# Performance work log

Hardware: AMD Instinct MI355X
Metric: run time of the kernel (lower is better)

Reference implementation:

```python
import jax, jax.numpy as jnp
import numpy as np

EPS = 1e-07

def setup_inputs() -> dict:
    key = jax.random.key(0)
    k1, k2, k3 = jax.random.split(key, 3)
    B, H, W = 32, 1024, 1024
    predictions = jax.random.uniform(k1, (B, 1, H, W), dtype=jnp.float32)
    # bboxes (x1,y1,x2,y2) normalized, with x1<x2 and y1<y2
    lo = jax.random.uniform(k2, (B, 2), dtype=jnp.float32) * 0.3        # x1,y1 in [0,0.3)
    hi = 0.6 + jax.random.uniform(k3, (B, 2), dtype=jnp.float32) * 0.4  # x2,y2 in [0.6,1.0)
    bboxes = jnp.concatenate([lo, hi], axis=1)  # [B,4]
    return {"predictions": predictions, "bboxes": bboxes}

def reference(predictions, bboxes):
    B, _, H, W = predictions.shape
    p = predictions[:, 0]  # [B,H,W]
    # int(bbox * dim) truncates; bbox >= 0 so floor matches torch's int()
    x1 = jnp.maximum(jnp.floor(bboxes[:, 0] * W).astype(jnp.int32), 0)
    y1 = jnp.maximum(jnp.floor(bboxes[:, 1] * H).astype(jnp.int32), 0)
    x2 = jnp.minimum(jnp.floor(bboxes[:, 2] * W).astype(jnp.int32), W)
    y2 = jnp.minimum(jnp.floor(bboxes[:, 3] * H).astype(jnp.int32), H)
    ys = jnp.arange(H, dtype=jnp.int32)[None, :, None]  # [1,H,1]
    xs = jnp.arange(W, dtype=jnp.int32)[None, None, :]  # [1,1,W]
    inside = ((ys >= y1[:, None, None]) & (ys < y2[:, None, None]) &
              (xs >= x1[:, None, None]) & (xs < x2[:, None, None]))  # [B,H,W]
    outside = ~inside
    per_pix = -jnp.log(1.0 - p + EPS)  # [B,H,W]
    cnt = jnp.sum(outside, axis=(1, 2)).astype(p.dtype)          # [B]
    s = jnp.sum(jnp.where(outside, per_pix, 0.0), axis=(1, 2))   # [B]
    per_sample = jnp.where(cnt > 0, s / jnp.maximum(cnt, 1.0), 0.0)
    return jnp.sum(per_sample) / B
```

## Files before the change

kernel.cpp:

```cpp
#include <hip/hip_runtime.h>
#include <math.h>

constexpr int B = 32;
constexpr int H = 1024;
constexpr int W = 1024;
constexpr int BPB  = 128;
constexpr int NBLK = B * BPB;
constexpr int RPB  = H / BPB;
constexpr int NTHREADS = 256;

__global__ __launch_bounds__(NTHREADS)
void partial_kernel(const float* __restrict__ pred,
                    const float* __restrict__ bboxes,
                    float* __restrict__ ws) {
    const int g   = blockIdx.x;
    const int b   = g & (B - 1);
    const int y0  = (g >> 5) * RPB;
    const int tid = threadIdx.x;

    const int x1 = max((int)floorf(bboxes[b * 4 + 0] * (float)W), 0);
    const int y1 = max((int)floorf(bboxes[b * 4 + 1] * (float)H), 0);
    const int x2 = min((int)floorf(bboxes[b * 4 + 2] * (float)W), W);
    const int y2 = min((int)floorf(bboxes[b * 4 + 3] * (float)H), H);

    const float area = (float)max(0, y2 - y1) * (float)max(0, x2 - x1);
    const float cnt  = (float)(H * W) - area;
    const float inv  = (cnt > 0.0f) ? (1.0f / fmaxf(cnt, 1.0f)) : 0.0f;

    const int nL   = (x1 + 3) >> 2;
    const int rS   = x2 >> 2;
    const int nAct = nL + (256 - rS);

    const float* base = pred + ((size_t)b << 20);

    float acc = 0.0f;
#pragma unroll
    for (int j = 0; j < RPB; ++j) {
        const int y = y0 + j;
        const bool yin = (y >= y1) && (y < y2);
        int c4;
        if (yin) {
            if (tid < nL)        c4 = tid;
            else if (tid < nAct) c4 = rS + (tid - nL);
            else continue;
        } else {
            c4 = tid;
        }

        const float4 v = *reinterpret_cast<const float4*>(
            base + ((size_t)y << 10) + (c4 << 2));
        const float pv[4] = {v.x, v.y, v.z, v.w};
#pragma unroll
        for (int k = 0; k < 4; ++k) {
            const int x = (c4 << 2) + k;
            const bool inside = yin && (x >= x1) && (x < x2);
            if (!inside) acc -= __logf(1.0f - pv[k] + 1e-7f);
        }
    }
    acc *= inv;

    for (int off = 32; off > 0; off >>= 1)
        acc += __shfl_down(acc, off, 64);
    __shared__ float s[NTHREADS / 64];
    const int wave = tid >> 6;
    if ((tid & 63) == 0) s[wave] = acc;
    __syncthreads();
    if (tid == 0)
        ws[g] = s[0] + s[1] + s[2] + s[3];
}

__global__ __launch_bounds__(NTHREADS)
void finalize_kernel(const float* __restrict__ ws, float* __restrict__ out) {
    const int tid = threadIdx.x;
    float t = 0.0f;
    const float* p = ws + (size_t)tid * (NBLK / NTHREADS);
#pragma unroll
    for (int i = 0; i < NBLK / NTHREADS; ++i) t += p[i];
    for (int off = 32; off > 0; off >>= 1)
        t += __shfl_down(t, off, 64);
    __shared__ float s[NTHREADS / 64];
    const int wave = tid >> 6;
    if ((tid & 63) == 0) s[wave] = t;
    __syncthreads();
    if (tid == 0)
        out[0] = (s[0] + s[1] + s[2] + s[3]) * (1.0f / (float)B);
}

extern "C" void kernel_launch(void* const* d_in, const int* in_sizes, int n_in,
                              void* d_out, int out_size, void* d_ws, size_t ws_size,
                              hipStream_t stream) {
    const float* pred   = (const float*)d_in[0];
    const float* bboxes = (const float*)d_in[1];
    float* out = (float*)d_out;
    float* ws  = (float*)d_ws;

    partial_kernel<<<NBLK, NTHREADS, 0, stream>>>(pred, bboxes, ws);
    finalize_kernel<<<1, NTHREADS, 0, stream>>>(ws, out);
}
```

Measured before the change: 24.84 us.

## Interleave rows per block and split loops into outside/inside bbox regions

```diff
diff --git a/kernel.cpp b/kernel.cpp
--- a/kernel.cpp
+++ b/kernel.cpp
@@ -4,18 +4,36 @@
 constexpr int B = 32;
 constexpr int H = 1024;
 constexpr int W = 1024;
-constexpr int BPB  = 128;
+constexpr int BPB  = 64;
+constexpr int ROWS = H / BPB;
 constexpr int NBLK = B * BPB;
-constexpr int RPB  = H / BPB;
 constexpr int NTHREADS = 256;
+constexpr int STR = BPB * W;
+
+__device__ __forceinline__ float row4(const float4 v) {
+    float s = 0.0f;
+    s -= __logf(1.0f - v.x + 1e-7f);
+    s -= __logf(1.0f - v.y + 1e-7f);
+    s -= __logf(1.0f - v.z + 1e-7f);
+    s -= __logf(1.0f - v.w + 1e-7f);
+    return s;
+}
+__device__ __forceinline__ float row4w(const float4 v, const float4 w) {
+    float s = 0.0f;
+    s -= w.x * __logf(1.0f - v.x + 1e-7f);
+    s -= w.y * __logf(1.0f - v.y + 1e-7f);
+    s -= w.z * __logf(1.0f - v.z + 1e-7f);
+    s -= w.w * __logf(1.0f - v.w + 1e-7f);
+    return s;
+}
 
 __global__ __launch_bounds__(NTHREADS)
 void partial_kernel(const float* __restrict__ pred,
                     const float* __restrict__ bboxes,
                     float* __restrict__ ws) {
     const int g   = blockIdx.x;
-    const int b   = g & (B - 1);
-    const int y0  = (g >> 5) * RPB;
+    const int b   = g >> 6;
+    const int blk = g & (BPB - 1);
     const int tid = threadIdx.x;
 
     const int x1 = max((int)floorf(bboxes[b * 4 + 0] * (float)W), 0);
@@ -27,43 +45,68 @@
     const float cnt  = (float)(H * W) - area;
     const float inv  = (cnt > 0.0f) ? (1.0f / fmaxf(cnt, 1.0f)) : 0.0f;
 
-    const int nL   = (x1 + 3) >> 2;
-    const int rS   = x2 >> 2;
-    const int nAct = nL + (256 - rS);
+    const int iLo = min(ROWS, max(0, (y1 - blk + 63) >> 6));
+    const int iHi = min(ROWS, max(iLo, (y2 - blk + 63) >> 6));
 
-    const float* base = pred + ((size_t)b << 20);
+    const float* base = pred + ((size_t)b << 20) + ((size_t)blk << 10);
+    const float* pO   = base + (tid << 2);
 
-    float acc = 0.0f;
-#pragma unroll
-    for (int j = 0; j < RPB; ++j) {
-        const int y = y0 + j;
-        const bool yin = (y >= y1) && (y < y2);
-        int c4;
-        if (yin) {
-            if (tid < nL)        c4 = tid;
-            else if (tid < nAct) c4 = rS + (tid - nL);
-            else continue;
-        } else {
-            c4 = tid;
+    float acc = 0.0f, acc2 = 0.0f;
+
+    {
+        int i = 0;
+        for (; i + 2 <= iLo; i += 2) {
+            const float4 va = *reinterpret_cast<const float4*>(pO + (size_t)i * STR);
+            const float4 vb = *reinterpret_cast<const float4*>(pO + (size_t)(i + 1) * STR);
+            acc += row4(va);
+            acc2 += row4(vb);
         }
-
-        const float4 v = *reinterpret_cast<const float4*>(
-            base + ((size_t)y << 10) + (c4 << 2));
-        const float pv[4] = {v.x, v.y, v.z, v.w};
-#pragma unroll
-        for (int k = 0; k < 4; ++k) {
-            const int x = (c4 << 2) + k;
-            const bool inside = yin && (x >= x1) && (x < x2);
-            if (!inside) acc -= __logf(1.0f - pv[k] + 1e-7f);
+        if (i < iLo)
+            acc += row4(*reinterpret_cast<const float4*>(pO + (size_t)i * STR));
+    }
+    {
+        int i = iHi;
+        for (; i + 2 <= ROWS; i += 2) {
+            const float4 va = *reinterpret_cast<const float4*>(pO + (size_t)i * STR);
+            const float4 vb = *reinterpret_cast<const float4*>(pO + (size_t)(i + 1) * STR);
+            acc += row4(va);
+            acc2 += row4(vb);
+        }
+        if (i < ROWS)
+            acc += row4(*reinterpret_cast<const float4*>(pO + (size_t)i * STR));
+    }
+    {
+        const int nL   = (x1 + 3) >> 2;
+        const int rS   = x2 >> 2;
+        const int nAct = nL + (256 - rS);
+        if (tid < nAct) {
+            const int c4 = (tid < nL) ? tid : (rS + tid - nL);
+            const int x0 = c4 << 2;
+            const float4 w = make_float4(
+                (x0 + 0 >= x1 && x0 + 0 < x2) ? 0.0f : 1.0f,
+                (x0 + 1 >= x1 && x0 + 1 < x2) ? 0.0f : 1.0f,
+                (x0 + 2 >= x1 && x0 + 2 < x2) ? 0.0f : 1.0f,
+                (x0 + 3 >= x1 && x0 + 3 < x2) ? 0.0f : 1.0f);
+            const float* pI = base + x0;
+            int i = iLo;
+            for (; i + 2 <= iHi; i += 2) {
+                const float4 va = *reinterpret_cast<const float4*>(pI + (size_t)i * STR);
+                const float4 vb = *reinterpret_cast<const float4*>(pI + (size_t)(i + 1) * STR);
+                acc += row4w(va, w);
+                acc2 += row4w(vb, w);
+            }
+            if (i < iHi)
+                acc += row4w(*reinterpret_cast<const float4*>(pI + (size_t)i * STR), w);
         }
     }
-    acc *= inv;
+
+    float t = (acc + acc2) * inv;
 
     for (int off = 32; off > 0; off >>= 1)
-        acc += __shfl_down(acc, off, 64);
+        t += __shfl_down(t, off, 64);
     __shared__ float s[NTHREADS / 64];
     const int wave = tid >> 6;
-    if ((tid & 63) == 0) s[wave] = acc;
+    if ((tid & 63) == 0) s[wave] = t;
     __syncthreads();
     if (tid == 0)
         ws[g] = s[0] + s[1] + s[2] + s[3];
```

New measurement: 21.23 us. 14.5% less time.
